# Kernel tuning notes

Measured on AMD Instinct MI355X. Metric: run time of the kernel, lower is better.

The kernel has to match this reference:

```python
import jax, jax.numpy as jnp
import numpy as np

B, H, W, C = 8, 128, 128, 192
G, K = 6, 3
K2 = K * K
GC = C // G
OFFSET_SCALE = 0.1
DN = ('NHWC', 'HWIO', 'NHWC')


def setup_inputs() -> dict:
    key = jax.random.key(0)
    ks = jax.random.split(key, 8)
    s = 1.0 / np.sqrt(C)
    return {
        'x': jax.random.normal(ks[0], (B, H, W, C), jnp.float32),
        'w_in': jax.random.normal(ks[1], (C, C), jnp.float32) * s,
        'b_in': jnp.zeros((C,), jnp.float32),
        'w_dw': jax.random.normal(ks[2], (3, 3, 1, C), jnp.float32) / 3.0,  # depthwise 3x3, HWIO
        'b_dw': jnp.zeros((C,), jnp.float32),
        'w_pw': jax.random.normal(ks[3], (1, 1, C, C), jnp.float32) * s,  # 1x1 conv
        'b_pw': jnp.zeros((C,), jnp.float32),
        'w_off': jax.random.normal(ks[4], (C, G * K2 * 2), jnp.float32) * 0.01,
        'b_off': jnp.zeros((G * K2 * 2,), jnp.float32),
        'w_mask': jax.random.normal(ks[5], (C, G * K2), jnp.float32) * 0.01,
        'b_mask': jnp.zeros((G * K2,), jnp.float32),
        'w_out': jax.random.normal(ks[6], (C, C), jnp.float32) * s,
        'b_out': jnp.zeros((C,), jnp.float32),
    }


def _deform_forward(x, w_in, b_in, w_dw, b_dw, w_pw, b_pw, w_off, b_off, w_mask, b_mask, w_out, b_out):
    x_proj = x @ w_in + b_in  # [B,H,W,C]

    # dw_conv: depthwise 3x3 -> SiLU -> 1x1 pointwise (all channels-last)
    xd = jax.lax.conv_general_dilated(x, w_dw, (1, 1), 'SAME', dimension_numbers=DN,
                                      feature_group_count=C) + b_dw
    xd = xd * jax.nn.sigmoid(xd)  # SiLU
    xd = jax.lax.conv_general_dilated(xd, w_pw, (1, 1), 'SAME', dimension_numbers=DN) + b_pw

    offsets = (xd @ w_off + b_off).reshape(B, H, W, G, K2, 2) * OFFSET_SCALE
    attn = jax.nn.softmax((xd @ w_mask + b_mask).reshape(B, H, W, G, K2), axis=-1)
    attn = jnp.nan_to_num(attn, nan=0.0)

    r = jnp.arange(-(K // 2), K // 2 + 1, dtype=jnp.float32)
    ref_grid = jnp.stack(jnp.meshgrid(r, r, indexing='ij'), -1).reshape(K2, 2)  # [K2,2]
    pos = ref_grid + offsets  # [B,H,W,G,K2,2]
    pos_h = jnp.clip(pos[..., 0] + jnp.arange(H, dtype=jnp.float32)[None, :, None, None, None], 0.0, H - 1)
    pos_w = jnp.clip(pos[..., 1] + jnp.arange(W, dtype=jnp.float32)[None, None, :, None, None], 0.0, W - 1)

    xg = x_proj.reshape(B, H * W, G, GC)

    def gather(hi, wi):
        idx = (hi * W + wi).reshape(B, H * W, G, 1)
        return jnp.take_along_axis(xg, idx, axis=1).reshape(B, H, W, G, GC)

    def tap(acc, inputs):
        ph, pw, a = inputs  # each [B,H,W,G]
        hf = jnp.clip(ph.astype(jnp.int32), 0, H - 1)
        wf = jnp.clip(pw.astype(jnp.int32), 0, W - 1)
        hc = jnp.minimum(hf + 1, H - 1)
        wc = jnp.minimum(wf + 1, W - 1)
        hw = ph - hf.astype(jnp.float32)
        ww = pw - wf.astype(jnp.float32)
        sampled = (gather(hf, wf) * ((1 - hw) * (1 - ww))[..., None]
                   + gather(hf, wc) * ((1 - hw) * ww)[..., None]
                   + gather(hc, wf) * (hw * (1 - ww))[..., None]
                   + gather(hc, wc) * (hw * ww)[..., None])
        return acc + sampled * a[..., None], None

    xs = (jnp.moveaxis(pos_h, -1, 0), jnp.moveaxis(pos_w, -1, 0), jnp.moveaxis(attn, -1, 0))
    out, _ = jax.lax.scan(tap, jnp.zeros((B, H, W, G, GC), x.dtype), xs)
    return out.reshape(B, H, W, C) @ w_out + b_out


def reference(x, w_in, b_in, w_dw, b_dw, w_pw, b_pw, w_off, b_off, w_mask, b_mask, w_out, b_out):
    return _deform_forward(x, w_in, b_in, w_dw, b_dw, w_pw, b_pw,
                           w_off, b_off, w_mask, b_mask, w_out, b_out)
```

## Files before the change

### kernel.cpp

```cpp
#include <hip/hip_runtime.h>
#include <hip/hip_bf16.h>

#define Bn 8
#define Hn 128
#define Wn 128
#define Cn 192
#define Gn 6
#define GCn 32
#define NPIX (Bn*Hn*Wn)

typedef __attribute__((ext_vector_type(8))) short v8s;
typedef __attribute__((ext_vector_type(4))) float v4f;
typedef __attribute__((ext_vector_type(2))) float v2f;
typedef __hip_bfloat16 bf16;

__device__ __forceinline__ float b2f(bf16 v){ return __bfloat162float(v); }
__device__ __forceinline__ float lo16(unsigned u){ return __uint_as_float(u << 16); }
__device__ __forceinline__ float hi16(unsigned u){ return __uint_as_float(u & 0xffff0000u); }
__device__ __forceinline__ v2f up2(unsigned u){
    return (v2f){ __uint_as_float(u << 16), __uint_as_float(u & 0xffff0000u) };
}

__global__ __launch_bounds__(256) void cvt_bf16(const float* __restrict__ in,
                                                bf16* __restrict__ out, long n)
{
    long base = ((long)blockIdx.x*256 + threadIdx.x)*8;
    if (base >= n) return;
    float v[8];
    *(float4*)(v)   = *(const float4*)(in + base);
    *(float4*)(v+4) = *(const float4*)(in + base + 4);
    bf16 o[8];
    #pragma unroll
    for (int j=0;j<8;j++) o[j] = __float2bfloat16(v[j]);
    *(uint4*)(out + base) = *(uint4*)o;
}

__global__ __launch_bounds__(256) void swizzle_w(const float* __restrict__ w,
                                                 bf16* __restrict__ out, int N)
{
    int idx = blockIdx.x*256 + threadIdx.x;
    int j = idx & 7, lane = (idx>>3)&63, ks = (idx>>9)%6, nt = idx/3072;
    int k = ks*32 + ((lane>>4)<<3) + j;
    int n = (nt<<4) + (lane&15);
    out[idx] = (n < N) ? __float2bfloat16(w[k*N + n]) : __float2bfloat16(0.0f);
}

__global__ __launch_bounds__(256) void swizzle_om(const float* __restrict__ woff,
        const float* __restrict__ wmask, const float* __restrict__ boff,
        const float* __restrict__ bmask, bf16* __restrict__ out, float* __restrict__ biascat)
{
    int idx = blockIdx.x*256 + threadIdx.x;
    if (idx < 192) {
        float bv = 0.0f;
        if (idx < 108) bv = boff[idx];
        else if (idx < 162) bv = bmask[idx-108];
        biascat[idx] = bv;
    }
    int j = idx & 7, lane = (idx>>3)&63, ks = (idx>>9)%6, nt = idx/3072;
    int k = ks*32 + ((lane>>4)<<3) + j;
    int n = (nt<<4) + (lane&15);
    float v = 0.0f;
    if (n < 108)      v = woff[k*108 + n];
    else if (n < 162) v = wmask[k*54 + (n-108)];
    out[idx] = __float2bfloat16(v);
}

__device__ __forceinline__ void store_out(bf16* p, float v){ *p = __float2bfloat16(v); }
__device__ __forceinline__ void store_out(float* p, float v){ *p = v; }

template<typename OutT>
__global__ __launch_bounds__(256, 2) void gemm6r(const bf16* __restrict__ A,
        const v8s* __restrict__ wfrag, const float* __restrict__ bias,
        OutT* __restrict__ Cmat, int Nreal, int Nstride)
{
    int tid = threadIdx.x;
    int wave = tid >> 6, lane = tid & 63;
    int q = lane >> 4, r = lane & 15;
    int n = blockIdx.x;
    int l = (n & 7) * 128 + (n >> 3);
    int yhalf = l & 1;
    int mt0 = l >> 1;
    const v8s* wsrc = wfrag + yhalf*(36*64) + lane;
    v8s breg[36];
    #pragma unroll
    for (int f=0; f<36; f++) breg[f] = wsrc[f*64];
    int col0 = yhalf*96;
    float bv[6];
    #pragma unroll
    for (int nt=0; nt<6; nt++) {
        int col = col0 + nt*16 + r;
        bv[nt] = (col < Nreal) ? bias[col] : 0.0f;
    }
    const int MT = NPIX/64;
    for (int mt = mt0; mt < MT; mt += 512) {
        const bf16* Ap = A + (size_t)(mt*64 + wave*16 + r)*Cn + q*8;
        v8s av[6];
        #pragma unroll
        for (int ks=0; ks<6; ks++) av[ks] = *(const v8s*)(Ap + ks*32);
        v4f acc[6];
        #pragma unroll
        for (int nt=0;nt<6;nt++) acc[nt] = (v4f){0.f,0.f,0.f,0.f};
        #pragma unroll
        for (int ks=0; ks<6; ks++)
            #pragma unroll
            for (int nt=0;nt<6;nt++)
                acc[nt] = __builtin_amdgcn_mfma_f32_16x16x32_bf16(
                              av[ks], breg[nt*6+ks], acc[nt], 0, 0, 0);
        int orow = mt*64 + wave*16 + q*4;
        #pragma unroll
        for (int nt=0;nt<6;nt++) {
            int col = col0 + nt*16 + r;
            if (col < Nreal) {
                #pragma unroll
                for (int i=0;i<4;i++)
                    store_out(&Cmat[(size_t)(orow+i)*Nstride + col], acc[nt][i] + bv[nt]);
            }
        }
    }
}

__global__ __launch_bounds__(256, 4) void dw_silu(const bf16* __restrict__ x,
        const bf16* __restrict__ wdwb, const float* __restrict__ bdw, bf16* __restrict__ out)
{
    int bid = blockIdx.x;
    int bsw = (bid & 7) * 768 + (bid >> 3);
    int idx = bsw*256 + threadIdx.x;
    int c16 = idx % 12; int pix = idx / 12;
    int b = pix >> 14; int hw = pix & 16383; int h = hw >> 7, w = hw & 127;
    int cb = c16*16;
    v2f acc2[8];
    #pragma unroll
    for (int j=0;j<8;j++) acc2[j] = (v2f){bdw[cb+2*j], bdw[cb+2*j+1]};
    #pragma unroll
    for (int dy=-1;dy<=1;dy++){
        int hh=h+dy; if ((unsigned)hh >= (unsigned)Hn) continue;
        #pragma unroll
        for (int dx=-1;dx<=1;dx++){
            int ww=w+dx; if ((unsigned)ww >= (unsigned)Wn) continue;
            const uint4* xp = (const uint4*)(x + ((size_t)((b<<14)+(hh<<7)+ww))*Cn + cb);
            const uint4* wp = (const uint4*)(wdwb + ((dy+1)*3+(dx+1))*Cn + cb);
            #pragma unroll
            for (int cs=0;cs<2;cs++){
                uint4 xu = xp[cs], wu = wp[cs];
                unsigned xa[4] = {xu.x,xu.y,xu.z,xu.w};
                unsigned wa[4] = {wu.x,wu.y,wu.z,wu.w};
                #pragma unroll
                for (int t=0;t<4;t++)
                    acc2[cs*4+t] += up2(xa[t]) * up2(wa[t]);
            }
        }
    }
    bf16 ov[16];
    #pragma unroll
    for (int j=0;j<8;j++){
        float v0 = acc2[j].x, v1 = acc2[j].y;
        ov[2*j]   = __float2bfloat16(v0 / (1.f + __expf(-v0)));
        ov[2*j+1] = __float2bfloat16(v1 / (1.f + __expf(-v1)));
    }
    uint4* op = (uint4*)(out + (size_t)pix*Cn + cb);
    op[0] = ((uint4*)ov)[0];
    op[1] = ((uint4*)ov)[1];
}


#define LOADTAP(K, S)                                                        \
  { float ph = (float)(h + (K)/3 - 1) + 0.1f*lo16(op[K]);                    \
    float pw = (float)(w + (K)%3 - 1) + 0.1f*hi16(op[K]);                    \
    ph = fminf(fmaxf(ph, 0.f), 127.f);                                       \
    pw = fminf(fmaxf(pw, 0.f), 127.f);                                       \
    int hf = (int)ph, wf = (int)pw;                                          \
    fh##S = ph - (float)hf; fw##S = pw - (float)wf;                          \
    int hc = min(hf+1,127), wc = min(wf+1,127);                              \
    const uint4* p00 = (const uint4*)(xb + ((hf<<7)+wf)*Cn);                 \
    const uint4* p01 = (const uint4*)(xb + ((hf<<7)+wc)*Cn);                 \
    const uint4* p10 = (const uint4*)(xb + ((hc<<7)+wf)*Cn);                 \
    const uint4* p11 = (const uint4*)(xb + ((hc<<7)+wc)*Cn);                 \
    S##00[0]=p00[0]; S##00[1]=p00[1]; S##01[0]=p01[0]; S##01[1]=p01[1];      \
    S##10[0]=p10[0]; S##10[1]=p10[1]; S##11[0]=p11[0]; S##11[1]=p11[1]; }

#define ACCTAP(K, S)                                                         \
  { float a = att[K];                                                        \
    float w00=(1.f-fh##S)*(1.f-fw##S)*a, w01=(1.f-fh##S)*fw##S*a,            \
          w10=fh##S*(1.f-fw##S)*a, w11=fh##S*fw##S*a;                        \
    _Pragma("unroll")                                                        \
    for (int cs=0;cs<2;cs++){                                                \
      unsigned u00[4]={S##00[cs].x,S##00[cs].y,S##00[cs].z,S##00[cs].w};     \
      unsigned u01[4]={S##01[cs].x,S##01[cs].y,S##01[cs].z,S##01[cs].w};     \
      unsigned u10[4]={S##10[cs].x,S##10[cs].y,S##10[cs].z,S##10[cs].w};     \
      unsigned u11[4]={S##11[cs].x,S##11[cs].y,S##11[cs].z,S##11[cs].w};     \
      _Pragma("unroll")                                                      \
      for (int t=0;t<4;t++)                                                  \
        acc2[cs*4+t] += up2(u00[t])*w00 + up2(u01[t])*w01                    \
                      + up2(u10[t])*w10 + up2(u11[t])*w11; } }

__global__ __launch_bounds__(256, 4) void deform_sample(const bf16* __restrict__ P,
        const bf16* __restrict__ OM, bf16* __restrict__ S)
{
    int bid = blockIdx.x;
    int bsw = (bid & 7) * 768 + (bid >> 3);
    int idx = bsw*256 + threadIdx.x;
    int half = idx & 1;
    int g = (idx >> 1) % 6;
    int pix = idx / 12;
    int b = pix >> 14; int hw = pix & 16383; int h = hw >> 7, w = hw & 127;
    const bf16* om = OM + (size_t)pix*162;
    const bf16* oml = om + 108 + g*9;
    const unsigned* ofp = (const unsigned*)(om + g*18);

    unsigned op[9];
    #pragma unroll
    for (int k=0;k<9;k++) op[k] = ofp[k];

    float att[9];
    float m = -1e30f;
    #pragma unroll
    for (int k=0;k<9;k++){ att[k] = b2f(oml[k]); m = fmaxf(m, att[k]); }
    float ssum = 0.f;
    #pragma unroll
    for (int k=0;k<9;k++){ att[k] = __expf(att[k]-m); ssum += att[k]; }
    float inv = 1.f/ssum;
    #pragma unroll
    for (int k=0;k<9;k++) att[k] *= inv;

    int chbase = g*GCn + half*16;
    const bf16* xb = P + ((((size_t)b) << 14))*Cn + chbase;

    v2f acc2[8];
    #pragma unroll
    for (int j=0;j<8;j++) acc2[j] = (v2f){0.f, 0.f};

    uint4 A00[2],A01[2],A10[2],A11[2]; float fhA,fwA;
    uint4 B00[2],B01[2],B10[2],B11[2]; float fhB,fwB;

    LOADTAP(0, A)
    LOADTAP(1, B)
    ACCTAP(0, A)  LOADTAP(2, A)
    ACCTAP(1, B)  LOADTAP(3, B)
    ACCTAP(2, A)  LOADTAP(4, A)
    ACCTAP(3, B)  LOADTAP(5, B)
    ACCTAP(4, A)  LOADTAP(6, A)
    ACCTAP(5, B)  LOADTAP(7, B)
    ACCTAP(6, A)  LOADTAP(8, A)
    ACCTAP(7, B)
    ACCTAP(8, A)

    bf16 ov[16];
    #pragma unroll
    for (int j=0;j<8;j++){
        ov[2*j]   = __float2bfloat16(acc2[j].x);
        ov[2*j+1] = __float2bfloat16(acc2[j].y);
    }
    uint4* sp = (uint4*)(S + (size_t)pix*Cn + chbase);
    sp[0] = ((uint4*)ov)[0];
    sp[1] = ((uint4*)ov)[1];
}

extern "C" void kernel_launch(void* const* d_in, const int* in_sizes, int n_in,
                              void* d_out, int out_size, void* d_ws, size_t ws_size,
                              hipStream_t stream)
{
    const float* x      = (const float*)d_in[0];
    const float* w_in   = (const float*)d_in[1];
    const float* b_in   = (const float*)d_in[2];
    const float* w_dw   = (const float*)d_in[3];
    const float* b_dw   = (const float*)d_in[4];
    const float* w_pw   = (const float*)d_in[5];
    const float* b_pw   = (const float*)d_in[6];
    const float* w_off  = (const float*)d_in[7];
    const float* b_off  = (const float*)d_in[8];
    const float* w_mask = (const float*)d_in[9];
    const float* b_mask = (const float*)d_in[10];
    const float* w_out  = (const float*)d_in[11];
    const float* b_out  = (const float*)d_in[12];
    float* out = (float*)d_out;

    char* ws = (char*)d_ws;
    size_t off = 0;
    auto carve = [&](size_t bytes)->char* {
        char* p = ws + off; off += (bytes + 255) & ~(size_t)255; return p; };
    bf16* XB  = (bf16*)carve((size_t)NPIX*Cn*2);
    bf16* P   = (bf16*)carve((size_t)NPIX*Cn*2);
    bf16* D   = (bf16*)carve((size_t)NPIX*Cn*2);
    bf16* OM  = (bf16*)carve((size_t)NPIX*162*2);
    bf16* wfI = (bf16*)carve(36864*2);
    bf16* wfP = (bf16*)carve(36864*2);
    bf16* wfO = (bf16*)carve(36864*2);
    bf16* wfM = (bf16*)carve(36864*2);
    float* bM = (float*)carve(192*4);
    bf16* WDW = (bf16*)carve(1728*2);

    dim3 blk(256);
    cvt_bf16<<<12288, blk, 0, stream>>>(x, XB, (long)NPIX*Cn);
    cvt_bf16<<<1,     blk, 0, stream>>>(w_dw, WDW, 1728);
    swizzle_w<<<144, blk, 0, stream>>>(w_in,  wfI, 192);
    swizzle_w<<<144, blk, 0, stream>>>(w_pw,  wfP, 192);
    swizzle_w<<<144, blk, 0, stream>>>(w_out, wfO, 192);
    swizzle_om<<<144, blk, 0, stream>>>(w_off, w_mask, b_off, b_mask, wfM, bM);

    gemm6r<bf16><<<1024, blk, 0, stream>>>(XB, (const v8s*)wfI, b_in, P, 192, 192);

    dw_silu<<<6144, blk, 0, stream>>>(XB, WDW, b_dw, D);

    bf16* X2 = XB;
    gemm6r<bf16><<<1024, blk, 0, stream>>>(D,  (const v8s*)wfP, b_pw, X2, 192, 192);
    gemm6r<bf16><<<1024, blk, 0, stream>>>(X2, (const v8s*)wfM, bM,  OM, 162, 162);

    deform_sample<<<6144, blk, 0, stream>>>(P, OM, D);

    gemm6r<float><<<1024, blk, 0, stream>>>(D, (const v8s*)wfO, b_out, out, 192, 192);
}
```

Baseline: 418.9 us.

## Fold pointwise conv into offset/mask weights, fuse x conversion into depthwise, retile GEMMs

Precomputes the product of the 1x1 pointwise weights with the offset and mask projection weights (and the matching biases), which removes one full-size GEMM and its intermediate buffer. The fp32-to-bf16 conversion of x now happens inside the depthwise SiLU kernel, which reads fp32 x directly, so a separate pass over x is gone. The GEMM is retiled to quarter-column blocks with fewer weight registers, allowing higher occupancy. Deform sampling switches to precomputed uint4 indexing and drops the softmax max-subtraction, which relies on the mask logits staying small to avoid overflow.

```diff
diff --git a/kernel.cpp b/kernel.cpp
--- a/kernel.cpp
+++ b/kernel.cpp
@@ -21,20 +21,6 @@
     return (v2f){ __uint_as_float(u << 16), __uint_as_float(u & 0xffff0000u) };
 }
 
-__global__ __launch_bounds__(256) void cvt_bf16(const float* __restrict__ in,
-                                                bf16* __restrict__ out, long n)
-{
-    long base = ((long)blockIdx.x*256 + threadIdx.x)*8;
-    if (base >= n) return;
-    float v[8];
-    *(float4*)(v)   = *(const float4*)(in + base);
-    *(float4*)(v+4) = *(const float4*)(in + base + 4);
-    bf16 o[8];
-    #pragma unroll
-    for (int j=0;j<8;j++) o[j] = __float2bfloat16(v[j]);
-    *(uint4*)(out + base) = *(uint4*)o;
-}
-
 __global__ __launch_bounds__(256) void swizzle_w(const float* __restrict__ w,
                                                  bf16* __restrict__ out, int N)
 {
@@ -45,31 +31,42 @@
     out[idx] = (n < N) ? __float2bfloat16(w[k*N + n]) : __float2bfloat16(0.0f);
 }
 
-__global__ __launch_bounds__(256) void swizzle_om(const float* __restrict__ woff,
-        const float* __restrict__ wmask, const float* __restrict__ boff,
+__global__ __launch_bounds__(256) void swizzle_omc(const float* __restrict__ wpw,
+        const float* __restrict__ woff, const float* __restrict__ wmask,
+        const float* __restrict__ bpw, const float* __restrict__ boff,
         const float* __restrict__ bmask, bf16* __restrict__ out, float* __restrict__ biascat)
 {
     int idx = blockIdx.x*256 + threadIdx.x;
+    int j = idx & 7, lane = (idx>>3)&63, ks = (idx>>9)%6, nt = idx/3072;
+    int k = ks*32 + ((lane>>4)<<3) + j;
+    int m = (nt<<4) + (lane&15);
+    float acc = 0.0f;
+    if (m < 162) {
+        const float* wrow = wpw + k*192;
+        for (int n=0; n<192; n++) {
+            float wc = (m < 108) ? woff[n*108 + m] : wmask[n*54 + (m-108)];
+            acc += wrow[n] * wc;
+        }
+    }
+    out[idx] = __float2bfloat16(acc);
     if (idx < 192) {
         float bv = 0.0f;
-        if (idx < 108) bv = boff[idx];
-        else if (idx < 162) bv = bmask[idx-108];
+        if (idx < 162) {
+            bv = (idx < 108) ? boff[idx] : bmask[idx-108];
+            for (int n=0; n<192; n++) {
+                float wc = (idx < 108) ? woff[n*108 + idx] : wmask[n*54 + (idx-108)];
+                bv += bpw[n] * wc;
+            }
+        }
         biascat[idx] = bv;
     }
-    int j = idx & 7, lane = (idx>>3)&63, ks = (idx>>9)%6, nt = idx/3072;
-    int k = ks*32 + ((lane>>4)<<3) + j;
-    int n = (nt<<4) + (lane&15);
-    float v = 0.0f;
-    if (n < 108)      v = woff[k*108 + n];
-    else if (n < 162) v = wmask[k*54 + (n-108)];
-    out[idx] = __float2bfloat16(v);
 }
 
 __device__ __forceinline__ void store_out(bf16* p, float v){ *p = __float2bfloat16(v); }
 __device__ __forceinline__ void store_out(float* p, float v){ *p = v; }
 
 template<typename OutT>
-__global__ __launch_bounds__(256, 2) void gemm6r(const bf16* __restrict__ A,
+__global__ __launch_bounds__(256, 4) void gemmq(const bf16* __restrict__ A,
         const v8s* __restrict__ wfrag, const float* __restrict__ bias,
         OutT* __restrict__ Cmat, int Nreal, int Nstride)
 {
@@ -77,38 +74,40 @@
     int wave = tid >> 6, lane = tid & 63;
     int q = lane >> 4, r = lane & 15;
     int n = blockIdx.x;
-    int l = (n & 7) * 128 + (n >> 3);
-    int yhalf = l & 1;
-    int mt0 = l >> 1;
-    const v8s* wsrc = wfrag + yhalf*(36*64) + lane;
-    v8s breg[36];
-    #pragma unroll
-    for (int f=0; f<36; f++) breg[f] = wsrc[f*64];
-    int col0 = yhalf*96;
-    float bv[6];
-    #pragma unroll
-    for (int nt=0; nt<6; nt++) {
+    int l = (n & 7) * 256 + (n >> 3);
+    int quarter = l & 3;
+    int mt0 = l >> 2;
+    const v8s* wsrc = wfrag + quarter*(18*64) + lane;
+    v8s breg[18];
+    #pragma unroll
+    for (int f=0; f<18; f++) breg[f] = wsrc[f*64];
+    int col0 = quarter*48;
+    float bv[3];
+    #pragma unroll
+    for (int nt=0; nt<3; nt++) {
         int col = col0 + nt*16 + r;
         bv[nt] = (col < Nreal) ? bias[col] : 0.0f;
     }
-    const int MT = NPIX/64;
-    for (int mt = mt0; mt < MT; mt += 512) {
+    for (int mt = mt0; mt < 2048; mt += 512) {
         const bf16* Ap = A + (size_t)(mt*64 + wave*16 + r)*Cn + q*8;
-        v8s av[6];
+        v4f acc[3];
         #pragma unroll
-        for (int ks=0; ks<6; ks++) av[ks] = *(const v8s*)(Ap + ks*32);
-        v4f acc[6];
+        for (int nt=0;nt<3;nt++) acc[nt] = (v4f){0.f,0.f,0.f,0.f};
         #pragma unroll
-        for (int nt=0;nt<6;nt++) acc[nt] = (v4f){0.f,0.f,0.f,0.f};
-        #pragma unroll
-        for (int ks=0; ks<6; ks++)
+        for (int kh=0; kh<2; kh++) {
+            v8s av[3];
             #pragma unroll
-            for (int nt=0;nt<6;nt++)
-                acc[nt] = __builtin_amdgcn_mfma_f32_16x16x32_bf16(
-                              av[ks], breg[nt*6+ks], acc[nt], 0, 0, 0);
+            for (int k2=0;k2<3;k2++) av[k2] = *(const v8s*)(Ap + (kh*3+k2)*32);
+            #pragma unroll
+            for (int k2=0;k2<3;k2++)
+                #pragma unroll
+                for (int nt=0;nt<3;nt++)
+                    acc[nt] = __builtin_amdgcn_mfma_f32_16x16x32_bf16(
+                                  av[k2], breg[nt*6 + kh*3 + k2], acc[nt], 0, 0, 0);
+        }
         int orow = mt*64 + wave*16 + q*4;
         #pragma unroll
-        for (int nt=0;nt<6;nt++) {
+        for (int nt=0;nt<3;nt++) {
             int col = col0 + nt*16 + r;
             if (col < Nreal) {
                 #pragma unroll
@@ -119,8 +118,9 @@
     }
 }
 
-__global__ __launch_bounds__(256, 4) void dw_silu(const bf16* __restrict__ x,
-        const bf16* __restrict__ wdwb, const float* __restrict__ bdw, bf16* __restrict__ out)
+__global__ __launch_bounds__(256, 4) void dw_silu(const float* __restrict__ x,
+        const float* __restrict__ wdw, const float* __restrict__ bdw,
+        bf16* __restrict__ xbout, bf16* __restrict__ out)
 {
     int bid = blockIdx.x;
     int bsw = (bid & 7) * 768 + (bid >> 3);
@@ -128,34 +128,38 @@
     int c16 = idx % 12; int pix = idx / 12;
     int b = pix >> 14; int hw = pix & 16383; int h = hw >> 7, w = hw & 127;
     int cb = c16*16;
-    v2f acc2[8];
-    #pragma unroll
-    for (int j=0;j<8;j++) acc2[j] = (v2f){bdw[cb+2*j], bdw[cb+2*j+1]};
+    float acc[16];
+    #pragma unroll
+    for (int j=0;j<16;j++) acc[j] = bdw[cb+j];
+    bf16 xc[16];
     #pragma unroll
     for (int dy=-1;dy<=1;dy++){
         int hh=h+dy; if ((unsigned)hh >= (unsigned)Hn) continue;
         #pragma unroll
         for (int dx=-1;dx<=1;dx++){
             int ww=w+dx; if ((unsigned)ww >= (unsigned)Wn) continue;
-            const uint4* xp = (const uint4*)(x + ((size_t)((b<<14)+(hh<<7)+ww))*Cn + cb);
-            const uint4* wp = (const uint4*)(wdwb + ((dy+1)*3+(dx+1))*Cn + cb);
+            const float4* xp = (const float4*)(x + ((size_t)((b<<14)+(hh<<7)+ww))*Cn + cb);
+            const float4* wp = (const float4*)(wdw + ((dy+1)*3+(dx+1))*Cn + cb);
+            float4 xv[4] = {xp[0], xp[1], xp[2], xp[3]};
+            float4 wv[4] = {wp[0], wp[1], wp[2], wp[3]};
+            const float* xf = (const float*)xv;
+            const float* wf = (const float*)wv;
             #pragma unroll
-            for (int cs=0;cs<2;cs++){
-                uint4 xu = xp[cs], wu = wp[cs];
-                unsigned xa[4] = {xu.x,xu.y,xu.z,xu.w};
-                unsigned wa[4] = {wu.x,wu.y,wu.z,wu.w};
+            for (int j=0;j<16;j++) acc[j] += xf[j]*wf[j];
+            if (dy==0 && dx==0) {
                 #pragma unroll
-                for (int t=0;t<4;t++)
-                    acc2[cs*4+t] += up2(xa[t]) * up2(wa[t]);
+                for (int j=0;j<16;j++) xc[j] = __float2bfloat16(xf[j]);
             }
         }
     }
+    uint4* xbp = (uint4*)(xbout + (size_t)pix*Cn + cb);
+    xbp[0] = ((uint4*)xc)[0];
+    xbp[1] = ((uint4*)xc)[1];
     bf16 ov[16];
     #pragma unroll
-    for (int j=0;j<8;j++){
-        float v0 = acc2[j].x, v1 = acc2[j].y;
-        ov[2*j]   = __float2bfloat16(v0 / (1.f + __expf(-v0)));
-        ov[2*j+1] = __float2bfloat16(v1 / (1.f + __expf(-v1)));
+    for (int j=0;j<16;j++){
+        float v = acc[j];
+        ov[j] = __float2bfloat16(v / (1.f + __expf(-v)));
     }
     uint4* op = (uint4*)(out + (size_t)pix*Cn + cb);
     op[0] = ((uint4*)ov)[0];
@@ -170,13 +174,14 @@
     pw = fminf(fmaxf(pw, 0.f), 127.f);                                       \
     int hf = (int)ph, wf = (int)pw;                                          \
     fh##S = ph - (float)hf; fw##S = pw - (float)wf;                          \
-    int hc = min(hf+1,127), wc = min(wf+1,127);                              \
-    const uint4* p00 = (const uint4*)(xb + ((hf<<7)+wf)*Cn);                 \
-    const uint4* p01 = (const uint4*)(xb + ((hf<<7)+wc)*Cn);                 \
-    const uint4* p10 = (const uint4*)(xb + ((hc<<7)+wf)*Cn);                 \
-    const uint4* p11 = (const uint4*)(xb + ((hc<<7)+wc)*Cn);                 \
-    S##00[0]=p00[0]; S##00[1]=p00[1]; S##01[0]=p01[0]; S##01[1]=p01[1];      \
-    S##10[0]=p10[0]; S##10[1]=p10[1]; S##11[0]=p11[0]; S##11[1]=p11[1]; }
+    int a00 = qbase + hf*3072 + wf*24;                                       \
+    int dh  = (hf < 127) ? 3072 : 0;                                         \
+    int dwq = (wf < 127) ? 24 : 0;                                           \
+    int a10 = a00 + dh;                                                      \
+    S##00[0]=P4[a00];      S##00[1]=P4[a00+1];                               \
+    S##01[0]=P4[a00+dwq];  S##01[1]=P4[a00+dwq+1];                           \
+    S##10[0]=P4[a10];      S##10[1]=P4[a10+1];                               \
+    S##11[0]=P4[a10+dwq];  S##11[1]=P4[a10+dwq+1]; }
 
 #define ACCTAP(K, S)                                                         \
   { float a = att[K];                                                        \
@@ -203,27 +208,24 @@
     int g = (idx >> 1) % 6;
     int pix = idx / 12;
     int b = pix >> 14; int hw = pix & 16383; int h = hw >> 7, w = hw & 127;
-    const bf16* om = OM + (size_t)pix*162;
-    const bf16* oml = om + 108 + g*9;
-    const unsigned* ofp = (const unsigned*)(om + g*18);
-
+
+    const unsigned* OMu = (const unsigned*)OM;
+    int omq = pix*81 + g*9;
     unsigned op[9];
     #pragma unroll
-    for (int k=0;k<9;k++) op[k] = ofp[k];
-
+    for (int k=0;k<9;k++) op[k] = OMu[omq + k];
+
+    int oml = pix*162 + 108 + g*9;
     float att[9];
-    float m = -1e30f;
-    #pragma unroll
-    for (int k=0;k<9;k++){ att[k] = b2f(oml[k]); m = fmaxf(m, att[k]); }
     float ssum = 0.f;
     #pragma unroll
-    for (int k=0;k<9;k++){ att[k] = __expf(att[k]-m); ssum += att[k]; }
+    for (int k=0;k<9;k++){ att[k] = __expf(b2f(OM[oml+k])); ssum += att[k]; }
     float inv = 1.f/ssum;
     #pragma unroll
     for (int k=0;k<9;k++) att[k] *= inv;
 
-    int chbase = g*GCn + half*16;
-    const bf16* xb = P + ((((size_t)b) << 14))*Cn + chbase;
+    const uint4* P4 = (const uint4*)P;
+    int qbase = b*393216 + (g<<2) + (half<<1);
 
     v2f acc2[8];
     #pragma unroll
@@ -250,9 +252,10 @@
         ov[2*j]   = __float2bfloat16(acc2[j].x);
         ov[2*j+1] = __float2bfloat16(acc2[j].y);
     }
-    uint4* sp = (uint4*)(S + (size_t)pix*Cn + chbase);
-    sp[0] = ((uint4*)ov)[0];
-    sp[1] = ((uint4*)ov)[1];
+    uint4* S4 = (uint4*)S;
+    int sidx = pix*24 + (g<<2) + (half<<1);
+    S4[sidx]   = ((uint4*)ov)[0];
+    S4[sidx+1] = ((uint4*)ov)[1];
 }
 
 extern "C" void kernel_launch(void* const* d_in, const int* in_sizes, int n_in,
@@ -283,29 +286,21 @@
     bf16* D   = (bf16*)carve((size_t)NPIX*Cn*2);
     bf16* OM  = (bf16*)carve((size_t)NPIX*162*2);
     bf16* wfI = (bf16*)carve(36864*2);
-    bf16* wfP = (bf16*)carve(36864*2);
     bf16* wfO = (bf16*)carve(36864*2);
     bf16* wfM = (bf16*)carve(36864*2);
     float* bM = (float*)carve(192*4);
-    bf16* WDW = (bf16*)carve(1728*2);
 
     dim3 blk(256);
-    cvt_bf16<<<12288, blk, 0, stream>>>(x, XB, (long)NPIX*Cn);
-    cvt_bf16<<<1,     blk, 0, stream>>>(w_dw, WDW, 1728);
     swizzle_w<<<144, blk, 0, stream>>>(w_in,  wfI, 192);
-    swizzle_w<<<144, blk, 0, stream>>>(w_pw,  wfP, 192);
     swizzle_w<<<144, blk, 0, stream>>>(w_out, wfO, 192);
-    swizzle_om<<<144, blk, 0, stream>>>(w_off, w_mask, b_off, b_mask, wfM, bM);
-
-    gemm6r<bf16><<<1024, blk, 0, stream>>>(XB, (const v8s*)wfI, b_in, P, 192, 192);
-
-    dw_silu<<<6144, blk, 0, stream>>>(XB, WDW, b_dw, D);
-
-    bf16* X2 = XB;
-    gemm6r<bf16><<<1024, blk, 0, stream>>>(D,  (const v8s*)wfP, b_pw, X2, 192, 192);
-    gemm6r<bf16><<<1024, blk, 0, stream>>>(X2, (const v8s*)wfM, bM,  OM, 162, 162);
+    swizzle_omc<<<144, blk, 0, stream>>>(w_pw, w_off, w_mask, b_pw, b_off, b_mask, wfM, bM);
+
+    dw_silu<<<6144, blk, 0, stream>>>(x, w_dw, b_dw, XB, D);
+
+    gemmq<bf16><<<2048, blk, 0, stream>>>(XB, (const v8s*)wfI, b_in, P, 192, 192);
+    gemmq<bf16><<<2048, blk, 0, stream>>>(D,  (const v8s*)wfM, bM,  OM, 162, 162);
 
     deform_sample<<<6144, blk, 0, stream>>>(P, OM, D);
 
-    gemm6r<float><<<1024, blk, 0, stream>>>(D, (const v8s*)wfO, b_out, out, 192, 192);
-}
+    gemmq<float><<<2048, blk, 0, stream>>>(D, (const v8s*)wfO, b_out, out, 192, 192);
+}
```

Result: slower. 526.2 us (+25.6%).
